# Kernel optimization log

Measured on AMD Instinct MI355X. Metric: run time of the kernel, lower is better.

The kernel has to match this reference:

```python
import jax, jax.numpy as jnp
import numpy as np

N, K, S, E = 8192, 15, 128, 24
H, A, HID, DEPTH, MIX = 8, 32, 512, 3, 10
RBF_MAX, RBF_K = 20.0, 16


def _norm(v):
    return v / (jnp.linalg.norm(v, axis=-1, keepdims=True) + 1e-8)


def orientation_frames(pos):
    # pos: [N,3] CA coords -> per-residue local rotation frames [N,3,3]
    u = _norm(pos[1:] - pos[:-1])
    b = _norm(u[:-1] - u[1:])
    n = _norm(jnp.cross(u[:-1], u[1:]))
    o = jnp.cross(b, n)
    R = jnp.stack([b, n, o], axis=-1)              # [N-2,3,3]
    return jnp.concatenate([R[:1], R, R[-1:]], 0)  # edge-pad to [N,3,3]


def rot_to_quat(R):
    m00, m11, m22 = R[..., 0, 0], R[..., 1, 1], R[..., 2, 2]
    def comp(t, a, b):
        return 0.5 * jnp.sqrt(jnp.maximum(1e-8, t)) * jnp.sign(a - b)
    qw = 0.5 * jnp.sqrt(jnp.maximum(1e-8, 1. + m00 + m11 + m22))
    qx = comp(1. + m00 - m11 - m22, R[..., 2, 1], R[..., 1, 2])
    qy = comp(1. - m00 + m11 - m22, R[..., 0, 2], R[..., 2, 0])
    qz = comp(1. - m00 - m11 + m22, R[..., 1, 0], R[..., 0, 1])
    return jnp.stack([qw, qx, qy, qz], axis=-1)


def rbf_expand(d):
    mu = jnp.linspace(0., RBF_MAX, RBF_K)
    sigma = RBF_MAX / RBF_K
    return jnp.exp(-((d[..., None] - mu) / sigma) ** 2)


def layer_norm(x, g, b):
    m = x.mean(-1, keepdims=True)
    v = ((x - m) ** 2).mean(-1, keepdims=True)
    return (x - m) / jnp.sqrt(v + 1e-5) * g + b


def edge_features(pos, R, structure):
    # Target features are roll-by-1 of self (as in the torch forward's
    # distances.roll(1, dims=0)); sources are k-NN neighbours [N,K].
    inds = jnp.arange(N, dtype=pos.dtype)
    pos_t, R_t, ind_t = jnp.roll(pos, 1, 0), jnp.roll(R, 1, 0), jnp.roll(inds, 1, 0)
    pos_s, R_s, ind_s = pos[structure], R[structure], inds[structure]
    dvec = pos_s - pos_t[:, None]                    # [N,K,3]
    dist = jnp.linalg.norm(dvec, axis=-1)            # [N,K]
    direction = jnp.einsum('nji,nkj->nki', R_t, _norm(dvec))
    R_rel = jnp.einsum('nji,nkjl->nkil', R_t, R_s)   # R_t^T R_s
    quat = rot_to_quat(R_rel)                        # [N,K,4]
    rel_ind = (ind_s - ind_t[:, None])[..., None] / 100.0
    return jnp.concatenate([rbf_expand(dist), direction, quat, rel_ind], -1)  # [N,K,24]


def _forward(angles, tertiary, structure, W_in, b_in, W_pre, b_pre,
             ln1_g, ln1_b, Wq, bq, Wk, bk, Wv, bv, Wo, bo, ln2_g, ln2_b,
             W1, b1, W2, b2, W3, b3, Ws, bs, Wc, bc,
             W_conc, b_conc, W_wt, b_wt, W_fac, b_fac):
    prev = jnp.roll(angles, 1, 0).at[0].set(0.)
    afeat = jnp.concatenate([jnp.sin(prev), jnp.cos(prev)], -1)   # [N,6]
    feats = afeat @ W_in + b_in                                   # [N,S]
    pos = tertiary[:, 1]                                          # CA coords [N,3]
    R = orientation_frames(pos)
    edges = edge_features(pos, R, structure)                      # [N,K,E]
    x = feats @ W_pre + b_pre
    for d in range(DEPTH):
        nx = layer_norm(x, ln1_g[d], ln1_b[d])
        q = (nx @ Wq[d] + bq[d]).reshape(N, H, A)
        kv_in = jnp.concatenate([nx[structure], edges], -1)       # [N,K,S+E]
        k = (kv_in @ Wk[d] + bk[d]).reshape(N, K, H, A)
        v = (kv_in @ Wv[d] + bv[d]).reshape(N, K, H, A)
        logits = jnp.einsum('nha,nkha->nkh', q, k) / np.sqrt(A)
        attn = jax.nn.softmax(logits, axis=1)                     # over neighbours
        att = jnp.einsum('nkh,nkha->nha', attn, v).reshape(N, H * A) @ Wo[d] + bo[d]
        x = x + att
        h = layer_norm(x, ln2_g[d], ln2_b[d])
        h = jax.nn.relu(h @ W1[d] + b1[d])
        h = jax.nn.relu(h @ W2[d] + b2[d])
        x = x + (h @ W3[d] + b3[d])
    enc = x
    mean = jnp.arctan2(enc @ Ws + bs, enc @ Wc + bc).reshape(N, 3, MIX)
    factor = enc @ W_fac + b_fac
    mean = mean.at[:, 1].add((factor[:, 0] * angles[:, 0])[:, None])
    mean = mean.at[:, 2].add((factor[:, 1] * angles[:, 0] + factor[:, 2] * angles[:, 1])[:, None])
    conc = 0.1 + 1000. * jax.nn.sigmoid(enc @ W_conc + b_conc).reshape(N, 3, MIX)
    weights = jax.nn.softmax(enc @ W_wt + b_wt, axis=-1)
    return weights, mean, conc


def setup_inputs() -> dict:
    key = jax.random.key(0)
    ks = iter(jax.random.split(key, 64))
    def lin(i, o):
        return (jax.random.normal(next(ks), (i, o), jnp.float32) / np.sqrt(i),
                jnp.zeros((o,), jnp.float32))
    def stack_lin(i, o):
        w = jax.random.normal(next(ks), (DEPTH, i, o), jnp.float32) / np.sqrt(i)
        return w, jnp.zeros((DEPTH, o), jnp.float32)
    inp = {}
    inp['angles'] = jax.random.normal(next(ks), (N, 3), jnp.float32) * 1.5
    inp['tertiary'] = jax.random.normal(next(ks), (N, 3, 3), jnp.float32) * 3.0
    inp['structure'] = jax.random.randint(next(ks), (N, K), 0, N)
    inp['subgraph'] = jax.random.randint(next(ks), (N,), 0, 4)
    inp['W_in'], inp['b_in'] = lin(6, S)
    inp['W_pre'], inp['b_pre'] = lin(S, S)
    inp['ln1_g'] = jnp.ones((DEPTH, S)); inp['ln1_b'] = jnp.zeros((DEPTH, S))
    inp['ln2_g'] = jnp.ones((DEPTH, S)); inp['ln2_b'] = jnp.zeros((DEPTH, S))
    inp['Wq'], inp['bq'] = stack_lin(S, H * A)
    inp['Wk'], inp['bk'] = stack_lin(S + E, H * A)
    inp['Wv'], inp['bv'] = stack_lin(S + E, H * A)
    inp['Wo'], inp['bo'] = stack_lin(H * A, S)
    inp['W1'], inp['b1'] = stack_lin(S, HID)
    inp['W2'], inp['b2'] = stack_lin(HID, HID)
    inp['W3'], inp['b3'] = stack_lin(HID, S)
    inp['Ws'], inp['bs'] = lin(S, 3 * MIX)
    inp['Wc'], inp['bc'] = lin(S, 3 * MIX)
    inp['W_conc'], inp['b_conc'] = lin(S, 3 * MIX)
    inp['W_wt'], inp['b_wt'] = lin(S, MIX)
    inp['W_fac'], inp['b_fac'] = lin(S, 3)
    return inp


def reference(angles, tertiary, structure, subgraph, W_in, b_in, W_pre, b_pre,
              ln1_g, ln1_b, Wq, bq, Wk, bk, Wv, bv, Wo, bo, ln2_g, ln2_b,
              W1, b1, W2, b2, W3, b3, Ws, bs, Wc, bc,
              W_conc, b_conc, W_wt, b_wt, W_fac, b_fac):
    return _forward(angles, tertiary, structure, W_in, b_in, W_pre, b_pre,
                    ln1_g, ln1_b, Wq, bq, Wk, bk, Wv, bv, Wo, bo, ln2_g, ln2_b,
                    W1, b1, W2, b2, W3, b3, Ws, bs, Wc, bc,
                    W_conc, b_conc, W_wt, b_wt, W_fac, b_fac)
```

## Files before the change

kernel.cpp:

```cpp
#include <hip/hip_runtime.h>
#include <hip/hip_bf16.h>
#include <stdint.h>

#define NRES 8192
#define KNB  15
#define SDIM 128
#define EDIM 24
#define HIDD 512
#define NH   8
#define QDIM 256
#define MIXN 10

typedef _Float16 f16;
typedef _Float16 f16x8 __attribute__((ext_vector_type(8)));
typedef _Float16 f16x4 __attribute__((ext_vector_type(4)));
typedef _Float16 f16x2 __attribute__((ext_vector_type(2)));
typedef float f32x4 __attribute__((ext_vector_type(4)));

#if __has_builtin(__builtin_amdgcn_fdot2)
#define FDOT2(a,b,c) __builtin_amdgcn_fdot2((a),(b),(c),false)
#else
#define FDOT2(a,b,c) ((c) + (float)(a).x*(float)(b).x + (float)(a).y*(float)(b).y)
#endif

struct F3 { float x, y, z; };
__device__ __forceinline__ F3 f3sub(F3 a, F3 b) { return {a.x-b.x, a.y-b.y, a.z-b.z}; }
__device__ __forceinline__ F3 f3cross(F3 a, F3 b) {
  return {a.y*b.z - a.z*b.y, a.z*b.x - a.x*b.z, a.x*b.y - a.y*b.x};
}
__device__ __forceinline__ F3 f3norm(F3 a) {
  float l = sqrtf(a.x*a.x + a.y*a.y + a.z*a.z) + 1e-8f;
  float r = 1.f / l;
  return {a.x*r, a.y*r, a.z*r};
}
__device__ __forceinline__ F3 ldpos(const float* p, int i) { return {p[i*3], p[i*3+1], p[i*3+2]}; }

__global__ void pos_kernel(const float* __restrict__ tert, float* __restrict__ pos) {
  int n = blockIdx.x * blockDim.x + threadIdx.x;
  if (n >= NRES) return;
  pos[n*3+0] = tert[n*9+3];
  pos[n*3+1] = tert[n*9+4];
  pos[n*3+2] = tert[n*9+5];
}

__global__ void frames_kernel(const float* __restrict__ pos, float* __restrict__ R) {
  int m = blockIdx.x * blockDim.x + threadIdx.x;
  if (m >= NRES) return;
  int s = m - 1; if (s < 0) s = 0; if (s > NRES-3) s = NRES-3;
  F3 p0 = ldpos(pos, s), p1 = ldpos(pos, s+1), p2 = ldpos(pos, s+2);
  F3 u0 = f3norm(f3sub(p1, p0));
  F3 u1 = f3norm(f3sub(p2, p1));
  F3 b  = f3norm(f3sub(u0, u1));
  F3 nn = f3norm(f3cross(u0, u1));
  F3 o  = f3cross(b, nn);
  float* r = R + m*9;
  r[0]=b.x; r[1]=nn.x; r[2]=o.x;
  r[3]=b.y; r[4]=nn.y; r[5]=o.y;
  r[6]=b.z; r[7]=nn.z; r[8]=o.z;
}

__device__ __forceinline__ float quat_comp(float t, float a, float b) {
  float s = (a > b) ? 1.f : ((a < b) ? -1.f : 0.f);
  return 0.5f * sqrtf(fmaxf(1e-8f, t)) * s;
}

__global__ void edges_kernel(const float* __restrict__ pos, const float* __restrict__ R,
                             const int* __restrict__ structure, f16* __restrict__ edges) {
  int id = blockIdx.x * blockDim.x + threadIdx.x;
  if (id >= NRES*KNB) return;
  int n = id / KNB;
  int tprev = (n - 1) & (NRES - 1);
  int sidx = structure[id];
  F3 pt = ldpos(pos, tprev), ps = ldpos(pos, sidx);
  F3 dv = f3sub(ps, pt);
  float dist = sqrtf(dv.x*dv.x + dv.y*dv.y + dv.z*dv.z);
  float rinv = 1.f / (dist + 1e-8f);
  F3 dh = {dv.x*rinv, dv.y*rinv, dv.z*rinv};
  float Rt[9], Rs[9];
#pragma unroll
  for (int i = 0; i < 9; i++) { Rt[i] = R[tprev*9+i]; Rs[i] = R[sidx*9+i]; }
  float dir[3];
#pragma unroll
  for (int i = 0; i < 3; i++) dir[i] = Rt[i]*dh.x + Rt[3+i]*dh.y + Rt[6+i]*dh.z;
  float Rr[9];
#pragma unroll
  for (int i = 0; i < 3; i++)
#pragma unroll
    for (int l = 0; l < 3; l++)
      Rr[i*3+l] = Rt[i]*Rs[l] + Rt[3+i]*Rs[3+l] + Rt[6+i]*Rs[6+l];
  float m00 = Rr[0], m11 = Rr[4], m22 = Rr[8];
  float qw = 0.5f * sqrtf(fmaxf(1e-8f, 1.f + m00 + m11 + m22));
  float qx = quat_comp(1.f + m00 - m11 - m22, Rr[7], Rr[5]);
  float qy = quat_comp(1.f - m00 + m11 - m22, Rr[2], Rr[6]);
  float qz = quat_comp(1.f - m00 - m11 + m22, Rr[3], Rr[1]);
  f16* e = edges + (size_t)id * EDIM;
#pragma unroll
  for (int j = 0; j < 16; j++) {
    float mu = (20.f / 15.f) * j;
    float zz = (dist - mu) * (1.f / 1.25f);
    e[j] = (f16)expf(-zz*zz);
  }
  e[16] = (f16)dir[0]; e[17] = (f16)dir[1]; e[18] = (f16)dir[2];
  e[19] = (f16)qw; e[20] = (f16)qx; e[21] = (f16)qy; e[22] = (f16)qz;
  e[23] = (f16)((float)(sidx - tprev) * 0.01f);
}

__global__ __launch_bounds__(128) void init_kernel(const float* __restrict__ angles,
    const float* __restrict__ W_in, const float* __restrict__ b_in,
    const float* __restrict__ W_pre, const float* __restrict__ b_pre, float* __restrict__ x) {
  int n = blockIdx.x, c = threadIdx.x;
  __shared__ float fs[128];
  float af[6];
  if (n == 0) { af[0]=af[1]=af[2]=0.f; af[3]=af[4]=af[5]=1.f; }
  else {
#pragma unroll
    for (int j = 0; j < 3; j++) {
      float p = angles[(n-1)*3 + j];
      af[j] = sinf(p); af[3+j] = cosf(p);
    }
  }
  float f = b_in[c];
#pragma unroll
  for (int j = 0; j < 6; j++) f += af[j] * W_in[j*SDIM + c];
  fs[c] = f;
  __syncthreads();
  float xv = b_pre[c];
  for (int j = 0; j < 128; j++) xv += fs[j] * W_pre[j*SDIM + c];
  x[(size_t)n*SDIM + c] = xv;
}

__global__ void convswz_kernel(const float* __restrict__ src, int srcLayerStride, int srcLd,
    int K, int N, f16* __restrict__ dst, int dstLayerHalves, int dstN, int colOff) {
  int d = blockIdx.y;
  const float* s = src + (size_t)d * srcLayerStride;
  f16* o = dst + (size_t)d * dstLayerHalves;
  for (int i = blockIdx.x*blockDim.x + threadIdx.x; i < K*N; i += gridDim.x*blockDim.x) {
    int k = i / N, n = i - k*N;
    o[((size_t)(k>>3)*dstN + colOff + n)*8 + (k&7)] = (f16)s[(size_t)k*srcLd + n];
  }
}

__global__ __launch_bounds__(128) void wcomb_kernel(const float* __restrict__ Wq,
    const float* __restrict__ bq, const float* __restrict__ Wk, const float* __restrict__ bk,
    f16* __restrict__ qkvw, float* __restrict__ b1024) {
  int blk = blockIdx.x;
  int d = blk >> 8, col = blk & 255;
  int k = threadIdx.x;
  float acc = 0.f, bacc = 0.f;
  if (col < 200) {
    int h = col / 25, jj = col % 25;
    const float* WkB = Wk + (size_t)d*(SDIM+EDIM)*QDIM + (size_t)SDIM*QDIM;
    const float* wqrow = Wq + (size_t)d*SDIM*QDIM + (size_t)k*QDIM;
    int r0 = h*32;
    for (int rr = 0; rr < 32; rr++) {
      int r = r0 + rr;
      float wd = (jj < 24) ? WkB[(size_t)jj*QDIM + r] : bk[d*QDIM + r];
      acc += wqrow[r] * wd;
      if (k == 0) bacc += bq[d*QDIM + r] * wd;
    }
  }
  qkvw[(size_t)d*131072 + ((size_t)(k>>3)*1024 + 768 + col)*8 + (k&7)] = (f16)acc;
  if (k == 0) b1024[d*1024 + 768 + col] = bacc;
}

__global__ void bias1024_kernel(const float* __restrict__ bq, float* __restrict__ out) {
  int i = blockIdx.x*blockDim.x + threadIdx.x;
  if (i >= 3*768) return;
  int d = i / 768, col = i - d*768;
  out[d*1024 + col] = (col < 256) ? bq[d*QDIM + col] : 0.f;
}

template<int MODE>
__global__ __launch_bounds__(256) void gemm_mfma(const f16* __restrict__ A,
    const f16* __restrict__ Bsw, const float* __restrict__ bias,
    void* __restrict__ Cv, int Kd, int Nd) {
  int w = blockIdx.x * 4 + (threadIdx.x >> 6);
  int lane = threadIdx.x & 63;
  int wm = w & 255, wn = w >> 8;
  int m0 = wm * 32, n0 = wn * 64;
  int r16 = lane & 15, qd = lane >> 4;
  f32x4 acc[2][4] = {};
  const f16* aBase = A + (size_t)(m0 + r16)*Kd + qd*8;
  for (int kc = 0; kc < Kd; kc += 32) {
    f16x8 af0 = *(const f16x8*)(aBase + kc);
    f16x8 af1 = *(const f16x8*)(aBase + (size_t)16*Kd + kc);
    const f16* bBase = Bsw + ((size_t)((kc>>3) + qd)*Nd + n0 + r16)*8;
    f16x8 bf[4];
#pragma unroll
    for (int nt = 0; nt < 4; nt++) bf[nt] = *(const f16x8*)(bBase + nt*16*8);
#pragma unroll
    for (int nt = 0; nt < 4; nt++) {
      acc[0][nt] = __builtin_amdgcn_mfma_f32_16x16x32_f16(af0, bf[nt], acc[0][nt], 0, 0, 0);
      acc[1][nt] = __builtin_amdgcn_mfma_f32_16x16x32_f16(af1, bf[nt], acc[1][nt], 0, 0, 0);
    }
  }
#pragma unroll
  for (int mt = 0; mt < 2; mt++) {
#pragma unroll
    for (int nt = 0; nt < 4; nt++) {
      int col = n0 + nt*16 + r16;
      float bj = bias ? bias[col] : 0.f;
#pragma unroll
      for (int r = 0; r < 4; r++) {
        int row = m0 + mt*16 + qd*4 + r;
        float v = acc[mt][nt][r] + bj;
        ((f16*)Cv)[(size_t)row*Nd + col] = (f16)fmaxf(v, 0.f);
      }
    }
  }
}

template<int MODE>
__global__ __launch_bounds__(256) void gemm_ln_mfma(const float* __restrict__ A,
    const float* __restrict__ lng, const float* __restrict__ lnb,
    const f16* __restrict__ Bsw, const float* __restrict__ bias,
    void* __restrict__ Cv, float* __restrict__ C2, int Nd) {
  int w = blockIdx.x * 4 + (threadIdx.x >> 6);
  int lane = threadIdx.x & 63;
  int wm = w & 255, wn = w >> 8;
  int m0 = wm * 32, n0 = wn * 64;
  int r16 = lane & 15, qd = lane >> 4;
  const float* r0p = A + (size_t)(m0 + r16)*SDIM + qd*8;
  const float* r1p = r0p + (size_t)16*SDIM;
  float4 a0[8], a1[8];
#pragma unroll
  for (int kc = 0; kc < 4; kc++) {
    a0[kc*2+0] = *(const float4*)(r0p + kc*32);
    a0[kc*2+1] = *(const float4*)(r0p + kc*32 + 4);
    a1[kc*2+0] = *(const float4*)(r1p + kc*32);
    a1[kc*2+1] = *(const float4*)(r1p + kc*32 + 4);
  }
  float s0 = 0.f, s1 = 0.f;
#pragma unroll
  for (int c = 0; c < 8; c++) {
    s0 += a0[c].x + a0[c].y + a0[c].z + a0[c].w;
    s1 += a1[c].x + a1[c].y + a1[c].z + a1[c].w;
  }
  s0 += __shfl_xor(s0, 16, 64); s0 += __shfl_xor(s0, 32, 64);
  s1 += __shfl_xor(s1, 16, 64); s1 += __shfl_xor(s1, 32, 64);
  float mean0 = s0 * (1.f/128.f), mean1 = s1 * (1.f/128.f);
  float v0 = 0.f, v1 = 0.f;
#pragma unroll
  for (int c = 0; c < 8; c++) {
    float d0x = a0[c].x-mean0, d0y = a0[c].y-mean0, d0z = a0[c].z-mean0, d0w = a0[c].w-mean0;
    v0 += d0x*d0x + d0y*d0y + d0z*d0z + d0w*d0w;
    float d1x = a1[c].x-mean1, d1y = a1[c].y-mean1, d1z = a1[c].z-mean1, d1w = a1[c].w-mean1;
    v1 += d1x*d1x + d1y*d1y + d1z*d1z + d1w*d1w;
  }
  v0 += __shfl_xor(v0, 16, 64); v0 += __shfl_xor(v0, 32, 64);
  v1 += __shfl_xor(v1, 16, 64); v1 += __shfl_xor(v1, 32, 64);
  float rs0 = rsqrtf(v0 * (1.f/128.f) + 1e-5f);
  float rs1 = rsqrtf(v1 * (1.f/128.f) + 1e-5f);
  f16x8 af0[4], af1[4];
#pragma unroll
  for (int kc = 0; kc < 4; kc++) {
    float4 g0 = *(const float4*)(lng + qd*8 + kc*32);
    float4 g1 = *(const float4*)(lng + qd*8 + kc*32 + 4);
    float4 bl0 = *(const float4*)(lnb + qd*8 + kc*32);
    float4 bl1 = *(const float4*)(lnb + qd*8 + kc*32 + 4);
    f16x8 f0, f1;
    f0[0] = (f16)((a0[kc*2].x  -mean0)*rs0*g0.x + bl0.x);
    f0[1] = (f16)((a0[kc*2].y  -mean0)*rs0*g0.y + bl0.y);
    f0[2] = (f16)((a0[kc*2].z  -mean0)*rs0*g0.z + bl0.z);
    f0[3] = (f16)((a0[kc*2].w  -mean0)*rs0*g0.w + bl0.w);
    f0[4] = (f16)((a0[kc*2+1].x-mean0)*rs0*g1.x + bl1.x);
    f0[5] = (f16)((a0[kc*2+1].y-mean0)*rs0*g1.y + bl1.y);
    f0[6] = (f16)((a0[kc*2+1].z-mean0)*rs0*g1.z + bl1.z);
    f0[7] = (f16)((a0[kc*2+1].w-mean0)*rs0*g1.w + bl1.w);
    f1[0] = (f16)((a1[kc*2].x  -mean1)*rs1*g0.x + bl0.x);
    f1[1] = (f16)((a1[kc*2].y  -mean1)*rs1*g0.y + bl0.y);
    f1[2] = (f16)((a1[kc*2].z  -mean1)*rs1*g0.z + bl0.z);
    f1[3] = (f16)((a1[kc*2].w  -mean1)*rs1*g0.w + bl0.w);
    f1[4] = (f16)((a1[kc*2+1].x-mean1)*rs1*g1.x + bl1.x);
    f1[5] = (f16)((a1[kc*2+1].y-mean1)*rs1*g1.y + bl1.y);
    f1[6] = (f16)((a1[kc*2+1].z-mean1)*rs1*g1.z + bl1.z);
    f1[7] = (f16)((a1[kc*2+1].w-mean1)*rs1*g1.w + bl1.w);
    af0[kc] = f0; af1[kc] = f1;
  }
  f32x4 acc[2][4] = {};
#pragma unroll
  for (int kc = 0; kc < 4; kc++) {
    const f16* bBase = Bsw + ((size_t)(kc*4 + qd)*Nd + n0 + r16)*8;
    f16x8 bf[4];
#pragma unroll
    for (int nt = 0; nt < 4; nt++) bf[nt] = *(const f16x8*)(bBase + nt*16*8);
#pragma unroll
    for (int nt = 0; nt < 4; nt++) {
      acc[0][nt] = __builtin_amdgcn_mfma_f32_16x16x32_f16(af0[kc], bf[nt], acc[0][nt], 0, 0, 0);
      acc[1][nt] = __builtin_amdgcn_mfma_f32_16x16x32_f16(af1[kc], bf[nt], acc[1][nt], 0, 0, 0);
    }
  }
#pragma unroll
  for (int mt = 0; mt < 2; mt++) {
#pragma unroll
    for (int nt = 0; nt < 4; nt++) {
      int col = n0 + nt*16 + r16;
      float bj = bias[col];
#pragma unroll
      for (int r = 0; r < 4; r++) {
        int row = m0 + mt*16 + qd*4 + r;
        float v = acc[mt][nt][r] + bj;
        if (MODE == 1) {
          ((f16*)Cv)[(size_t)row*Nd + col] = (f16)fmaxf(v, 0.f);
        } else {
          int third = col >> 8, cl = col & 255;
          if (third < 3)
            ((f16*)Cv)[(size_t)third*NRES*QDIM + (size_t)row*QDIM + cl] = (f16)v;
          else
            C2[(size_t)row*256 + cl] = v;
        }
      }
    }
  }
}

__global__ __launch_bounds__(256) void gemm_mfma16(const f16* __restrict__ A,
    const f16* __restrict__ Bsw, const float* __restrict__ bias,
    float* __restrict__ C, int Kd, int Nd) {
  int w = blockIdx.x * 4 + (threadIdx.x >> 6);
  int lane = threadIdx.x & 63;
  int wm = w & 511, wn = w >> 9;
  int m0 = wm * 16, n0 = wn * 64;
  int r16 = lane & 15, qd = lane >> 4;
  f32x4 acc[4] = {};
  const f16* aBase = A + (size_t)(m0 + r16)*Kd + qd*8;
  for (int kc = 0; kc < Kd; kc += 32) {
    f16x8 af = *(const f16x8*)(aBase + kc);
    const f16* bBase = Bsw + ((size_t)((kc>>3) + qd)*Nd + n0 + r16)*8;
#pragma unroll
    for (int nt = 0; nt < 4; nt++) {
      f16x8 bf = *(const f16x8*)(bBase + nt*16*8);
      acc[nt] = __builtin_amdgcn_mfma_f32_16x16x32_f16(af, bf, acc[nt], 0, 0, 0);
    }
  }
#pragma unroll
  for (int nt = 0; nt < 4; nt++) {
    int col = n0 + nt*16 + r16;
    float bj = bias[col];
#pragma unroll
    for (int r = 0; r < 4; r++) {
      int row = m0 + qd*4 + r;
      C[(size_t)row*Nd + col] += acc[nt][r] + bj;
    }
  }
}

__global__ __launch_bounds__(256) void attn_kernel(const f16* __restrict__ q,
    const f16* __restrict__ pk, const f16* __restrict__ pv,
    const f16* __restrict__ edges, const int* __restrict__ structure,
    const float* __restrict__ qW, const float* __restrict__ WvB,
    const float* __restrict__ bv, f16* __restrict__ att) {
  int t = threadIdx.x;
  int n = blockIdx.x*4 + (t >> 6);
  int lane = t & 63;
  int h = lane >> 3, i = lane & 7, base = h << 3;

  int s[KNB];
#pragma unroll
  for (int kk = 0; kk < KNB; kk++) s[kk] = structure[n*KNB + kk];
  const f16x4* pk4 = (const f16x4*)pk;
  const f16x4* pv4 = (const f16x4*)pv;
  f16x4 pks[KNB], pvs[KNB];
#pragma unroll
  for (int kk = 0; kk < KNB; kk++) pks[kk] = pk4[(size_t)s[kk]*64 + lane];
#pragma unroll
  for (int kk = 0; kk < KNB; kk++) pvs[kk] = pv4[(size_t)s[kk]*64 + lane];
  f16x4 q4 = ((const f16x4*)q)[(size_t)n*64 + lane];

  const float* qwr = qW + (size_t)n*256 + h*25;
  float qbias = qwr[24];
  float elA = qbias, elB = qbias;
  {
    const f16x2* eA = (const f16x2*)(edges + (size_t)n*KNB*EDIM + i*EDIM);
#pragma unroll
    for (int j2 = 0; j2 < 12; j2++) {
      f16x2 e2 = eA[j2];
      elA += qwr[2*j2]*(float)e2.x + qwr[2*j2+1]*(float)e2.y;
    }
  }
  if (i < 7) {
    const f16x2* eB = (const f16x2*)(edges + (size_t)n*KNB*EDIM + (i+8)*EDIM);
#pragma unroll
    for (int j2 = 0; j2 < 12; j2++) {
      f16x2 e2 = eB[j2];
      elB += qwr[2*j2]*(float)e2.x + qwr[2*j2+1]*(float)e2.y;
    }
  }

  float dot[KNB];
  f16x2 qlo; qlo.x = q4.x; qlo.y = q4.y;
  f16x2 qhi; qhi.x = q4.z; qhi.y = q4.w;
#pragma unroll
  for (int kk = 0; kk < KNB; kk++) {
    f16x2 plo; plo.x = pks[kk].x; plo.y = pks[kk].y;
    f16x2 phi; phi.x = pks[kk].z; phi.y = pks[kk].w;
    float p = FDOT2(qlo, plo, 0.f);
    p = FDOT2(qhi, phi, p);
    p += __shfl_xor(p, 4, 64);
    p += __shfl_xor(p, 2, 64);
    p += __shfl_xor(p, 1, 64);
    dot[kk] = p;
  }

  float logit[KNB];
#pragma unroll
  for (int kk = 0; kk < 8; kk++) {
    float el = __shfl(elA, base + kk, 64);
    logit[kk] = (dot[kk] + el) * 0.17677669529663687f;
  }
#pragma unroll
  for (int kk = 8; kk < KNB; kk++) {
    float el = __shfl(elB, base + (kk - 8), 64);
    logit[kk] = (dot[kk] + el) * 0.17677669529663687f;
  }

  float mx = -1e30f;
#pragma unroll
  for (int kk = 0; kk < KNB; kk++) mx = fmaxf(mx, logit[kk]);
  float attw[KNB]; float sum = 0.f;
#pragma unroll
  for (int kk = 0; kk < KNB; kk++) { attw[kk] = expf(logit[kk] - mx); sum += attw[kk]; }
  float inv = 1.f / sum;
#pragma unroll
  for (int kk = 0; kk < KNB; kk++) attw[kk] *= inv;

  float4 o = ((const float4*)bv)[lane];
#pragma unroll
  for (int kk = 0; kk < KNB; kk++) {
    float a = attw[kk];
    o.x += a * (float)pvs[kk].x;
    o.y += a * (float)pvs[kk].y;
    o.z += a * (float)pvs[kk].z;
    o.w += a * (float)pvs[kk].w;
  }

  const f16* ebase = edges + (size_t)n*KNB*EDIM;
  float ew0 = 0.f, ew1 = 0.f, ew2 = 0.f;
#pragma unroll
  for (int kk = 0; kk < KNB; kk++) {
    float a = attw[kk];
    ew0 += a * (float)ebase[kk*EDIM + 3*i + 0];
    ew1 += a * (float)ebase[kk*EDIM + 3*i + 1];
    ew2 += a * (float)ebase[kk*EDIM + 3*i + 2];
  }

#pragma unroll
  for (int src = 0; src < 8; src++) {
    float w0 = __shfl(ew0, base + src, 64);
    float w1 = __shfl(ew1, base + src, 64);
    float w2 = __shfl(ew2, base + src, 64);
    float4 wv0 = ((const float4*)(WvB + (size_t)(3*src + 0)*QDIM))[lane];
    float4 wv1 = ((const float4*)(WvB + (size_t)(3*src + 1)*QDIM))[lane];
    float4 wv2 = ((const float4*)(WvB + (size_t)(3*src + 2)*QDIM))[lane];
    o.x += w0*wv0.x + w1*wv1.x + w2*wv2.x;
    o.y += w0*wv0.y + w1*wv1.y + w2*wv2.y;
    o.z += w0*wv0.z + w1*wv1.z + w2*wv2.z;
    o.w += w0*wv0.w + w1*wv1.w + w2*wv2.w;
  }

  f16x4 ov; ov.x = (f16)o.x; ov.y = (f16)o.y; ov.z = (f16)o.z; ov.w = (f16)o.w;
  ((f16x4*)att)[(size_t)n*64 + lane] = ov;
}

__global__ __launch_bounds__(128) void head_kernel(const float* __restrict__ enc,
    const float* Ws, const float* bs, const float* Wc, const float* bc,
    const float* Wconc, const float* bconc, const float* Wwt, const float* bwt,
    const float* Wfac, const float* bfac, const float* __restrict__ angles, float* __restrict__ out) {
  int n = blockIdx.x, t = threadIdx.x;
  __shared__ float es[128];
  __shared__ float outs[103];
  es[t] = enc[(size_t)n*SDIM + t];
  __syncthreads();
  const float* W = nullptr; const float* bb = nullptr; int col = 0, nc = 0;
  if (t < 30)       { W = Ws;    bb = bs;    col = t;       nc = 30; }
  else if (t < 60)  { W = Wc;    bb = bc;    col = t - 30;  nc = 30; }
  else if (t < 90)  { W = Wconc; bb = bconc; col = t - 60;  nc = 30; }
  else if (t < 100) { W = Wwt;   bb = bwt;   col = t - 90;  nc = 10; }
  else if (t < 103) { W = Wfac;  bb = bfac;  col = t - 100; nc = 3;  }
  if (W) {
    float acc = bb[col];
    for (int j = 0; j < 128; j++) acc += es[j] * W[j*nc + col];
    outs[t] = acc;
  }
  __syncthreads();
  if (t < MIXN) {
    float mx = -1e30f;
    for (int m = 0; m < MIXN; m++) mx = fmaxf(mx, outs[90 + m]);
    float sum = 0.f;
    for (int m = 0; m < MIXN; m++) sum += expf(outs[90 + m] - mx);
    out[(size_t)n*MIXN + t] = expf(outs[90 + t] - mx) / sum;
  }
  if (t < 30) {
    int j = t / 10;
    float v = atan2f(outs[t], outs[30 + t]);
    float a0 = angles[n*3 + 0], a1 = angles[n*3 + 1];
    if (j == 1) v += outs[100] * a0;
    if (j == 2) v += outs[101] * a0 + outs[102] * a1;
    out[(size_t)NRES*MIXN + (size_t)n*30 + t] = v;
    float z = outs[60 + t];
    float sg = 1.f / (1.f + expf(-z));
    out[(size_t)NRES*MIXN + (size_t)NRES*30 + (size_t)n*30 + t] = 0.1f + 1000.f * sg;
  }
}

extern "C" void kernel_launch(void* const* d_in, const int* in_sizes, int n_in,
                              void* d_out, int out_size, void* d_ws, size_t ws_size,
                              hipStream_t stream) {
  const float* angles   = (const float*)d_in[0];
  const float* tertiary = (const float*)d_in[1];
  const int*   structure = (const int*)d_in[2];
  const float* W_in  = (const float*)d_in[4];  const float* b_in  = (const float*)d_in[5];
  const float* W_pre = (const float*)d_in[6];  const float* b_pre = (const float*)d_in[7];
  const float* ln1_g = (const float*)d_in[8];  const float* ln1_b = (const float*)d_in[9];
  const float* ln2_g = (const float*)d_in[10]; const float* ln2_b = (const float*)d_in[11];
  const float* Wq = (const float*)d_in[12]; const float* bq = (const float*)d_in[13];
  const float* Wk = (const float*)d_in[14]; const float* bk = (const float*)d_in[15];
  const float* Wv = (const float*)d_in[16]; const float* bv = (const float*)d_in[17];
  const float* Wo = (const float*)d_in[18]; const float* bo = (const float*)d_in[19];
  const float* W1 = (const float*)d_in[20]; const float* b1 = (const float*)d_in[21];
  const float* W2 = (const float*)d_in[22]; const float* b2 = (const float*)d_in[23];
  const float* W3 = (const float*)d_in[24]; const float* b3 = (const float*)d_in[25];
  const float* Ws = (const float*)d_in[26]; const float* bs = (const float*)d_in[27];
  const float* Wc = (const float*)d_in[28]; const float* bc = (const float*)d_in[29];
  const float* Wconc = (const float*)d_in[30]; const float* bconc = (const float*)d_in[31];
  const float* Wwt = (const float*)d_in[32]; const float* bwt = (const float*)d_in[33];
  const float* Wfac = (const float*)d_in[34]; const float* bfac = (const float*)d_in[35];

  char* wsb = (char*)d_ws;
  float* pos   = (float*)(wsb + 0);
  float* Rm    = (float*)(wsb + 98304);
  f16*   edg_h = (f16*)  (wsb + 393216);
  float* x     = (float*)(wsb + 6291456);
  f16*   att_h = (f16*)  (wsb + 12582912);
  f16*   qh    = (f16*)  (wsb + 16777216);
  f16*   pkh   = (f16*)  (wsb + 20971520);
  f16*   pvh   = (f16*)  (wsb + 25165824);
  f16*   h1h   = (f16*)  (wsb + 29360128);
  f16*   h2h   = (f16*)  (wsb + 37748736);
  f16*   qkvw  = (f16*)  (wsb + 46137344);
  f16*   w1w   = (f16*)  (wsb + 46923776);
  f16*   w2w   = (f16*)  (wsb + 47316992);
  f16*   w3w   = (f16*)  (wsb + 48889856);
  f16*   wow   = (f16*)  (wsb + 49283072);
  float* b1024 = (float*)(wsb + 49479680);
  float* qWb   = (float*)(wsb + 49491968);

  pos_kernel<<<dim3((NRES+255)/256), dim3(256), 0, stream>>>(tertiary, pos);
  frames_kernel<<<dim3((NRES+255)/256), dim3(256), 0, stream>>>(pos, Rm);
  edges_kernel<<<dim3((NRES*KNB+255)/256), dim3(256), 0, stream>>>(pos, Rm, structure, edg_h);
  init_kernel<<<dim3(NRES), dim3(128), 0, stream>>>(angles, W_in, b_in, W_pre, b_pre, x);

  convswz_kernel<<<dim3(64,3), 256, 0, stream>>>(Wq, SDIM*QDIM, QDIM, 128, 256, qkvw, 131072, 1024, 0);
  convswz_kernel<<<dim3(64,3), 256, 0, stream>>>(Wk, (SDIM+EDIM)*QDIM, QDIM, 128, 256, qkvw, 131072, 1024, 256);
  convswz_kernel<<<dim3(64,3), 256, 0, stream>>>(Wv, (SDIM+EDIM)*QDIM, QDIM, 128, 256, qkvw, 131072, 1024, 512);
  convswz_kernel<<<dim3(64,3), 256, 0, stream>>>(W1, SDIM*HIDD, HIDD, 128, 512, w1w, 65536, 512, 0);
  convswz_kernel<<<dim3(64,3), 256, 0, stream>>>(W2, HIDD*HIDD, HIDD, 512, 512, w2w, 262144, 512, 0);
  convswz_kernel<<<dim3(64,3), 256, 0, stream>>>(W3, HIDD*SDIM, SDIM, 512, 128, w3w, 65536, 128, 0);
  convswz_kernel<<<dim3(64,3), 256, 0, stream>>>(Wo, QDIM*SDIM, SDIM, 256, 128, wow, 32768, 128, 0);
  wcomb_kernel<<<768, 128, 0, stream>>>(Wq, bq, Wk, bk, qkvw, b1024);
  bias1024_kernel<<<9, 256, 0, stream>>>(bq, b1024);

  for (int d = 0; d < 3; ++d) {
    const float* WvD = Wv + (size_t)d*(SDIM+EDIM)*QDIM;
    gemm_ln_mfma<3><<<1024, 256, 0, stream>>>(x, ln1_g + d*SDIM, ln1_b + d*SDIM,
        qkvw + (size_t)d*131072, b1024 + d*1024, qh, qWb, 1024);
    attn_kernel<<<dim3(NRES/4), dim3(256), 0, stream>>>(qh, pkh, pvh, edg_h, structure,
        qWb, WvD + (size_t)SDIM*QDIM, bv + d*QDIM, att_h);
    gemm_mfma16<<<256, 256, 0, stream>>>(att_h, wow + (size_t)d*32768, bo + d*SDIM, x, 256, 128);
    gemm_ln_mfma<1><<<512, 256, 0, stream>>>(x, ln2_g + d*SDIM, ln2_b + d*SDIM,
        w1w + (size_t)d*65536, b1 + d*HIDD, h1h, nullptr, 512);
    gemm_mfma<1><<<512, 256, 0, stream>>>(h1h, w2w + (size_t)d*262144, b2 + d*HIDD, h2h, 512, 512);
    gemm_mfma16<<<256, 256, 0, stream>>>(h2h, w3w + (size_t)d*65536, b3 + d*SDIM, x, 512, 128);
  }

  head_kernel<<<dim3(NRES), dim3(128), 0, stream>>>(x, Ws, bs, Wc, bc, Wconc, bconc,
      Wwt, bwt, Wfac, bfac, angles, (float*)d_out);
}
```

Measured before the change: 504.7 us.

## Fuse FFN three GEMMs into one kernel and merge setup kernels

Replaces the three FFN launches (LN+W1, W2, W3 with residual add) with one kernel per 16-row tile that keeps the h1 and h2 intermediates in shared memory instead of round-tripping them through global memory. It also merges the seven weight-swizzle launches into one 3D-grid launch, folds the bias setup into wcomb, and drops the pos kernel by reading positions straight from tertiary. The aim is to cut global traffic for the 512-wide hidden activations and reduce launch count. In exchange, each block now re-streams the full W2 from global or cache with only 16 rows of reuse and has lower parallelism per block. In-place x read and write is kept safe by the per-row tile ownership.

```diff
diff --git a/kernel.cpp b/kernel.cpp
--- a/kernel.cpp
+++ b/kernel.cpp
@@ -33,21 +33,15 @@
   float r = 1.f / l;
   return {a.x*r, a.y*r, a.z*r};
 }
-__device__ __forceinline__ F3 ldpos(const float* p, int i) { return {p[i*3], p[i*3+1], p[i*3+2]}; }
-
-__global__ void pos_kernel(const float* __restrict__ tert, float* __restrict__ pos) {
-  int n = blockIdx.x * blockDim.x + threadIdx.x;
-  if (n >= NRES) return;
-  pos[n*3+0] = tert[n*9+3];
-  pos[n*3+1] = tert[n*9+4];
-  pos[n*3+2] = tert[n*9+5];
-}
-
-__global__ void frames_kernel(const float* __restrict__ pos, float* __restrict__ R) {
+__device__ __forceinline__ F3 ldter(const float* t, int i) {
+  return {t[i*9+3], t[i*9+4], t[i*9+5]};
+}
+
+__global__ void frames_kernel(const float* __restrict__ tert, float* __restrict__ R) {
   int m = blockIdx.x * blockDim.x + threadIdx.x;
   if (m >= NRES) return;
   int s = m - 1; if (s < 0) s = 0; if (s > NRES-3) s = NRES-3;
-  F3 p0 = ldpos(pos, s), p1 = ldpos(pos, s+1), p2 = ldpos(pos, s+2);
+  F3 p0 = ldter(tert, s), p1 = ldter(tert, s+1), p2 = ldter(tert, s+2);
   F3 u0 = f3norm(f3sub(p1, p0));
   F3 u1 = f3norm(f3sub(p2, p1));
   F3 b  = f3norm(f3sub(u0, u1));
@@ -64,14 +58,14 @@
   return 0.5f * sqrtf(fmaxf(1e-8f, t)) * s;
 }
 
-__global__ void edges_kernel(const float* __restrict__ pos, const float* __restrict__ R,
+__global__ void edges_kernel(const float* __restrict__ tert, const float* __restrict__ R,
                              const int* __restrict__ structure, f16* __restrict__ edges) {
   int id = blockIdx.x * blockDim.x + threadIdx.x;
   if (id >= NRES*KNB) return;
   int n = id / KNB;
   int tprev = (n - 1) & (NRES - 1);
   int sidx = structure[id];
-  F3 pt = ldpos(pos, tprev), ps = ldpos(pos, sidx);
+  F3 pt = ldter(tert, tprev), ps = ldter(tert, sidx);
   F3 dv = f3sub(ps, pt);
   float dist = sqrtf(dv.x*dv.x + dv.y*dv.y + dv.z*dv.z);
   float rinv = 1.f / (dist + 1e-8f);
@@ -129,14 +123,17 @@
   x[(size_t)n*SDIM + c] = xv;
 }
 
-__global__ void convswz_kernel(const float* __restrict__ src, int srcLayerStride, int srcLd,
-    int K, int N, f16* __restrict__ dst, int dstLayerHalves, int dstN, int colOff) {
-  int d = blockIdx.y;
-  const float* s = src + (size_t)d * srcLayerStride;
-  f16* o = dst + (size_t)d * dstLayerHalves;
-  for (int i = blockIdx.x*blockDim.x + threadIdx.x; i < K*N; i += gridDim.x*blockDim.x) {
-    int k = i / N, n = i - k*N;
-    o[((size_t)(k>>3)*dstN + colOff + n)*8 + (k&7)] = (f16)s[(size_t)k*srcLd + n];
+struct SwzJob { const float* src; int srcStride, srcLd, K, N; size_t dstOff; int dstLayerHalves, dstN, colOff; };
+struct SwzJobs { SwzJob j[7]; };
+__global__ void convswz_all(SwzJobs jobs, char* __restrict__ wsb) {
+  SwzJob jb = jobs.j[blockIdx.y];
+  int d = blockIdx.z;
+  const float* s = jb.src + (size_t)d * jb.srcStride;
+  f16* o = (f16*)(wsb + jb.dstOff) + (size_t)d * jb.dstLayerHalves;
+  int tot = jb.K * jb.N;
+  for (int i = blockIdx.x*blockDim.x + threadIdx.x; i < tot; i += gridDim.x*blockDim.x) {
+    int k = i / jb.N, n = i - k*jb.N;
+    o[((size_t)(k>>3)*jb.dstN + jb.colOff + n)*8 + (k&7)] = (f16)s[(size_t)k*jb.srcLd + n];
   }
 }
 
@@ -160,53 +157,11 @@
     }
   }
   qkvw[(size_t)d*131072 + ((size_t)(k>>3)*1024 + 768 + col)*8 + (k&7)] = (f16)acc;
-  if (k == 0) b1024[d*1024 + 768 + col] = bacc;
-}
-
-__global__ void bias1024_kernel(const float* __restrict__ bq, float* __restrict__ out) {
-  int i = blockIdx.x*blockDim.x + threadIdx.x;
-  if (i >= 3*768) return;
-  int d = i / 768, col = i - d*768;
-  out[d*1024 + col] = (col < 256) ? bq[d*QDIM + col] : 0.f;
-}
-
-template<int MODE>
-__global__ __launch_bounds__(256) void gemm_mfma(const f16* __restrict__ A,
-    const f16* __restrict__ Bsw, const float* __restrict__ bias,
-    void* __restrict__ Cv, int Kd, int Nd) {
-  int w = blockIdx.x * 4 + (threadIdx.x >> 6);
-  int lane = threadIdx.x & 63;
-  int wm = w & 255, wn = w >> 8;
-  int m0 = wm * 32, n0 = wn * 64;
-  int r16 = lane & 15, qd = lane >> 4;
-  f32x4 acc[2][4] = {};
-  const f16* aBase = A + (size_t)(m0 + r16)*Kd + qd*8;
-  for (int kc = 0; kc < Kd; kc += 32) {
-    f16x8 af0 = *(const f16x8*)(aBase + kc);
-    f16x8 af1 = *(const f16x8*)(aBase + (size_t)16*Kd + kc);
-    const f16* bBase = Bsw + ((size_t)((kc>>3) + qd)*Nd + n0 + r16)*8;
-    f16x8 bf[4];
-#pragma unroll
-    for (int nt = 0; nt < 4; nt++) bf[nt] = *(const f16x8*)(bBase + nt*16*8);
-#pragma unroll
-    for (int nt = 0; nt < 4; nt++) {
-      acc[0][nt] = __builtin_amdgcn_mfma_f32_16x16x32_f16(af0, bf[nt], acc[0][nt], 0, 0, 0);
-      acc[1][nt] = __builtin_amdgcn_mfma_f32_16x16x32_f16(af1, bf[nt], acc[1][nt], 0, 0, 0);
-    }
-  }
-#pragma unroll
-  for (int mt = 0; mt < 2; mt++) {
-#pragma unroll
-    for (int nt = 0; nt < 4; nt++) {
-      int col = n0 + nt*16 + r16;
-      float bj = bias ? bias[col] : 0.f;
-#pragma unroll
-      for (int r = 0; r < 4; r++) {
-        int row = m0 + mt*16 + qd*4 + r;
-        float v = acc[mt][nt][r] + bj;
-        ((f16*)Cv)[(size_t)row*Nd + col] = (f16)fmaxf(v, 0.f);
-      }
-    }
+  if (k == 0) {
+    b1024[d*1024 + col]       = bq[d*QDIM + col];
+    b1024[d*1024 + 256 + col] = 0.f;
+    b1024[d*1024 + 512 + col] = 0.f;
+    b1024[d*1024 + 768 + col] = bacc;
   }
 }
 
@@ -345,6 +300,123 @@
   }
 }
 
+__global__ __launch_bounds__(256) void ffn_kernel(const float* __restrict__ xin,
+    const float* __restrict__ lng, const float* __restrict__ lnb,
+    const f16* __restrict__ w1sw, const float* __restrict__ b1,
+    const f16* __restrict__ w2sw, const float* __restrict__ b2,
+    const f16* __restrict__ w3sw, const float* __restrict__ b3,
+    float* __restrict__ xout) {
+  __shared__ f16 h1s[16][520];
+  __shared__ f16 h2s[16][520];
+  int wv = threadIdx.x >> 6;
+  int lane = threadIdx.x & 63;
+  int m0 = blockIdx.x * 16;
+  int r16 = lane & 15, qd = lane >> 4;
+
+  const float* rp = xin + (size_t)(m0 + r16)*SDIM + qd*8;
+  float4 a0[8];
+#pragma unroll
+  for (int kc = 0; kc < 4; kc++) {
+    a0[kc*2+0] = *(const float4*)(rp + kc*32);
+    a0[kc*2+1] = *(const float4*)(rp + kc*32 + 4);
+  }
+  float s0 = 0.f;
+#pragma unroll
+  for (int c = 0; c < 8; c++) s0 += a0[c].x + a0[c].y + a0[c].z + a0[c].w;
+  s0 += __shfl_xor(s0, 16, 64); s0 += __shfl_xor(s0, 32, 64);
+  float mean0 = s0 * (1.f/128.f);
+  float v0 = 0.f;
+#pragma unroll
+  for (int c = 0; c < 8; c++) {
+    float dx = a0[c].x-mean0, dy = a0[c].y-mean0, dz = a0[c].z-mean0, dw = a0[c].w-mean0;
+    v0 += dx*dx + dy*dy + dz*dz + dw*dw;
+  }
+  v0 += __shfl_xor(v0, 16, 64); v0 += __shfl_xor(v0, 32, 64);
+  float rs0 = rsqrtf(v0 * (1.f/128.f) + 1e-5f);
+  f16x8 af[4];
+#pragma unroll
+  for (int kc = 0; kc < 4; kc++) {
+    float4 g0 = *(const float4*)(lng + qd*8 + kc*32);
+    float4 g1 = *(const float4*)(lng + qd*8 + kc*32 + 4);
+    float4 bl0 = *(const float4*)(lnb + qd*8 + kc*32);
+    float4 bl1 = *(const float4*)(lnb + qd*8 + kc*32 + 4);
+    f16x8 f0;
+    f0[0] = (f16)((a0[kc*2].x  -mean0)*rs0*g0.x + bl0.x);
+    f0[1] = (f16)((a0[kc*2].y  -mean0)*rs0*g0.y + bl0.y);
+    f0[2] = (f16)((a0[kc*2].z  -mean0)*rs0*g0.z + bl0.z);
+    f0[3] = (f16)((a0[kc*2].w  -mean0)*rs0*g0.w + bl0.w);
+    f0[4] = (f16)((a0[kc*2+1].x-mean0)*rs0*g1.x + bl1.x);
+    f0[5] = (f16)((a0[kc*2+1].y-mean0)*rs0*g1.y + bl1.y);
+    f0[6] = (f16)((a0[kc*2+1].z-mean0)*rs0*g1.z + bl1.z);
+    f0[7] = (f16)((a0[kc*2+1].w-mean0)*rs0*g1.w + bl1.w);
+    af[kc] = f0;
+  }
+  {
+    f32x4 acc[8] = {};
+#pragma unroll
+    for (int kc = 0; kc < 4; kc++) {
+      const f16* bBase = w1sw + ((size_t)(kc*4 + qd)*HIDD + wv*128 + r16)*8;
+#pragma unroll
+      for (int nt = 0; nt < 8; nt++) {
+        f16x8 bf = *(const f16x8*)(bBase + nt*16*8);
+        acc[nt] = __builtin_amdgcn_mfma_f32_16x16x32_f16(af[kc], bf, acc[nt], 0, 0, 0);
+      }
+    }
+#pragma unroll
+    for (int nt = 0; nt < 8; nt++) {
+      int col = wv*128 + nt*16 + r16;
+      float bj = b1[col];
+#pragma unroll
+      for (int r = 0; r < 4; r++)
+        h1s[qd*4 + r][col] = (f16)fmaxf(acc[nt][r] + bj, 0.f);
+    }
+  }
+  __syncthreads();
+  {
+    f32x4 acc[8] = {};
+    for (int kc = 0; kc < 16; kc++) {
+      f16x8 a = *(const f16x8*)&h1s[r16][qd*8 + kc*32];
+      const f16* bBase = w2sw + ((size_t)(kc*4 + qd)*HIDD + wv*128 + r16)*8;
+#pragma unroll
+      for (int nt = 0; nt < 8; nt++) {
+        f16x8 bf = *(const f16x8*)(bBase + nt*16*8);
+        acc[nt] = __builtin_amdgcn_mfma_f32_16x16x32_f16(a, bf, acc[nt], 0, 0, 0);
+      }
+    }
+#pragma unroll
+    for (int nt = 0; nt < 8; nt++) {
+      int col = wv*128 + nt*16 + r16;
+      float bj = b2[col];
+#pragma unroll
+      for (int r = 0; r < 4; r++)
+        h2s[qd*4 + r][col] = (f16)fmaxf(acc[nt][r] + bj, 0.f);
+    }
+  }
+  __syncthreads();
+  {
+    f32x4 acc[2] = {};
+    for (int kc = 0; kc < 16; kc++) {
+      f16x8 a = *(const f16x8*)&h2s[r16][qd*8 + kc*32];
+      const f16* bBase = w3sw + ((size_t)(kc*4 + qd)*SDIM + wv*32 + r16)*8;
+#pragma unroll
+      for (int nt = 0; nt < 2; nt++) {
+        f16x8 bf = *(const f16x8*)(bBase + nt*16*8);
+        acc[nt] = __builtin_amdgcn_mfma_f32_16x16x32_f16(a, bf, acc[nt], 0, 0, 0);
+      }
+    }
+#pragma unroll
+    for (int nt = 0; nt < 2; nt++) {
+      int col = wv*32 + nt*16 + r16;
+      float bj = b3[col];
+#pragma unroll
+      for (int r = 0; r < 4; r++) {
+        int row = m0 + qd*4 + r;
+        xout[(size_t)row*SDIM + col] += acc[nt][r] + bj;
+      }
+    }
+  }
+}
+
 __global__ __launch_bounds__(256) void attn_kernel(const f16* __restrict__ q,
     const f16* __restrict__ pk, const f16* __restrict__ pv,
     const f16* __restrict__ edges, const int* __restrict__ structure,
@@ -527,38 +599,40 @@
   const float* Wfac = (const float*)d_in[34]; const float* bfac = (const float*)d_in[35];
 
   char* wsb = (char*)d_ws;
-  float* pos   = (float*)(wsb + 0);
-  float* Rm    = (float*)(wsb + 98304);
-  f16*   edg_h = (f16*)  (wsb + 393216);
-  float* x     = (float*)(wsb + 6291456);
-  f16*   att_h = (f16*)  (wsb + 12582912);
-  f16*   qh    = (f16*)  (wsb + 16777216);
-  f16*   pkh   = (f16*)  (wsb + 20971520);
-  f16*   pvh   = (f16*)  (wsb + 25165824);
-  f16*   h1h   = (f16*)  (wsb + 29360128);
-  f16*   h2h   = (f16*)  (wsb + 37748736);
-  f16*   qkvw  = (f16*)  (wsb + 46137344);
-  f16*   w1w   = (f16*)  (wsb + 46923776);
-  f16*   w2w   = (f16*)  (wsb + 47316992);
-  f16*   w3w   = (f16*)  (wsb + 48889856);
-  f16*   wow   = (f16*)  (wsb + 49283072);
-  float* b1024 = (float*)(wsb + 49479680);
-  float* qWb   = (float*)(wsb + 49491968);
-
-  pos_kernel<<<dim3((NRES+255)/256), dim3(256), 0, stream>>>(tertiary, pos);
-  frames_kernel<<<dim3((NRES+255)/256), dim3(256), 0, stream>>>(pos, Rm);
-  edges_kernel<<<dim3((NRES*KNB+255)/256), dim3(256), 0, stream>>>(pos, Rm, structure, edg_h);
+  float* Rm    = (float*)(wsb + 0);
+  f16*   edg_h = (f16*)  (wsb + 294912);
+  float* x     = (float*)(wsb + 6193152);
+  f16*   att_h = (f16*)  (wsb + 10387456);
+  f16*   qh    = (f16*)  (wsb + 14581760);
+  f16*   pkh   = (f16*)  (wsb + 18776064);
+  f16*   pvh   = (f16*)  (wsb + 22970368);
+  size_t qkvwOff = 27164672;
+  size_t w1wOff  = 27951104;
+  size_t w2wOff  = 28344320;
+  size_t w3wOff  = 29917184;
+  size_t wowOff  = 30310400;
+  f16*   qkvw  = (f16*)(wsb + qkvwOff);
+  f16*   w1w   = (f16*)(wsb + w1wOff);
+  f16*   w2w   = (f16*)(wsb + w2wOff);
+  f16*   w3w   = (f16*)(wsb + w3wOff);
+  f16*   wow   = (f16*)(wsb + wowOff);
+  float* b1024 = (float*)(wsb + 30507008);
+  float* qWb   = (float*)(wsb + 30519296);
+
+  frames_kernel<<<dim3((NRES+255)/256), dim3(256), 0, stream>>>(tertiary, Rm);
+  edges_kernel<<<dim3((NRES*KNB+255)/256), dim3(256), 0, stream>>>(tertiary, Rm, structure, edg_h);
   init_kernel<<<dim3(NRES), dim3(128), 0, stream>>>(angles, W_in, b_in, W_pre, b_pre, x);
 
-  convswz_kernel<<<dim3(64,3), 256, 0, stream>>>(Wq, SDIM*QDIM, QDIM, 128, 256, qkvw, 131072, 1024, 0);
-  convswz_kernel<<<dim3(64,3), 256, 0, stream>>>(Wk, (SDIM+EDIM)*QDIM, QDIM, 128, 256, qkvw, 131072, 1024, 256);
-  convswz_kernel<<<dim3(64,3), 256, 0, stream>>>(Wv, (SDIM+EDIM)*QDIM, QDIM, 128, 256, qkvw, 131072, 1024, 512);
-  convswz_kernel<<<dim3(64,3), 256, 0, stream>>>(W1, SDIM*HIDD, HIDD, 128, 512, w1w, 65536, 512, 0);
-  convswz_kernel<<<dim3(64,3), 256, 0, stream>>>(W2, HIDD*HIDD, HIDD, 512, 512, w2w, 262144, 512, 0);
-  convswz_kernel<<<dim3(64,3), 256, 0, stream>>>(W3, HIDD*SDIM, SDIM, 512, 128, w3w, 65536, 128, 0);
-  convswz_kernel<<<dim3(64,3), 256, 0, stream>>>(Wo, QDIM*SDIM, SDIM, 256, 128, wow, 32768, 128, 0);
+  SwzJobs jobs;
+  jobs.j[0] = { Wq, SDIM*QDIM,        QDIM, 128, 256, qkvwOff, 131072, 1024, 0   };
+  jobs.j[1] = { Wk, (SDIM+EDIM)*QDIM, QDIM, 128, 256, qkvwOff, 131072, 1024, 256 };
+  jobs.j[2] = { Wv, (SDIM+EDIM)*QDIM, QDIM, 128, 256, qkvwOff, 131072, 1024, 512 };
+  jobs.j[3] = { W1, SDIM*HIDD, HIDD, 128, 512, w1wOff, 65536,  512, 0 };
+  jobs.j[4] = { W2, HIDD*HIDD, HIDD, 512, 512, w2wOff, 262144, 512, 0 };
+  jobs.j[5] = { W3, HIDD*SDIM, SDIM, 512, 128, w3wOff, 65536,  128, 0 };
+  jobs.j[6] = { Wo, QDIM*SDIM, SDIM, 256, 128, wowOff, 32768,  128, 0 };
+  convswz_all<<<dim3(64, 7, 3), dim3(256), 0, stream>>>(jobs, wsb);
   wcomb_kernel<<<768, 128, 0, stream>>>(Wq, bq, Wk, bk, qkvw, b1024);
-  bias1024_kernel<<<9, 256, 0, stream>>>(bq, b1024);
 
   for (int d = 0; d < 3; ++d) {
     const float* WvD = Wv + (size_t)d*(SDIM+EDIM)*QDIM;
@@ -567,10 +641,10 @@
     attn_kernel<<<dim3(NRES/4), dim3(256), 0, stream>>>(qh, pkh, pvh, edg_h, structure,
         qWb, WvD + (size_t)SDIM*QDIM, bv + d*QDIM, att_h);
     gemm_mfma16<<<256, 256, 0, stream>>>(att_h, wow + (size_t)d*32768, bo + d*SDIM, x, 256, 128);
-    gemm_ln_mfma<1><<<512, 256, 0, stream>>>(x, ln2_g + d*SDIM, ln2_b + d*SDIM,
-        w1w + (size_t)d*65536, b1 + d*HIDD, h1h, nullptr, 512);
-    gemm_mfma<1><<<512, 256, 0, stream>>>(h1h, w2w + (size_t)d*262144, b2 + d*HIDD, h2h, 512, 512);
-    gemm_mfma16<<<256, 256, 0, stream>>>(h2h, w3w + (size_t)d*65536, b3 + d*SDIM, x, 512, 128);
+    ffn_kernel<<<dim3(NRES/16), dim3(256), 0, stream>>>(x, ln2_g + d*SDIM, ln2_b + d*SDIM,
+        w1w + (size_t)d*65536, b1 + d*HIDD,
+        w2w + (size_t)d*262144, b2 + d*HIDD,
+        w3w + (size_t)d*65536, b3 + d*SDIM, x);
   }
 
   head_kernel<<<dim3(NRES), dim3(128), 0, stream>>>(x, Ws, bs, Wc, bc, Wconc, bconc,
```

Result: faster. 439.4 us (-12.9%).
